# Kernel tuning notes

Measured on AMD Instinct MI355X. Metric: run time of the kernel, lower is better.

Reference implementation:

```python
import jax, jax.numpy as jnp
import numpy as np
from jax import lax

N_FFT = 1024
N_FREQ = N_FFT // 2 + 1  # 513
BATCH = 32
SAMPLES = 480000
HOP = 256


def setup_inputs() -> dict:
    key = jax.random.key(0)
    kx, kwin = jax.random.split(key)
    x = jax.random.normal(kx, (BATCH, 1, SAMPLES), dtype=jnp.float32)
    n = jnp.arange(N_FFT, dtype=jnp.float32)
    # standard rfft angular frequencies: w_k = 2*pi*k / N
    w = 2.0 * jnp.pi * jnp.arange(N_FREQ, dtype=jnp.float32) / N_FFT
    # Hann window (periodic), as typically used for STFT
    window = 0.5 - 0.5 * jnp.cos(2.0 * jnp.pi * jnp.arange(N_FFT, dtype=jnp.float32) / N_FFT)
    return {"x": x, "n": n, "w": w, "window": window, "hop_size": HOP, "power": 1}


def _create_dft_matrices(n, w, window):
    # temp[f, t] = w_f * n_t
    temp = w[:, None] * n[None, :]              # [n_freq, n_fft]
    Fr = jnp.cos(temp)
    Fi = -jnp.sin(temp)
    if window is not None:
        Fr = window * Fr
        Fi = window * Fi
    # conv1d weights: [out_ch=n_freq, in_ch=1, kernel=n_fft]
    return Fr[:, None, :], Fi[:, None, :]


def reference(x, n, w, window, hop_size, power):
    DFTr, DFTi = _create_dft_matrices(n, w, window)
    dn = ("NCH", "OIH", "NCH")
    real_x = lax.conv_general_dilated(x, DFTr, (hop_size,), "VALID", dimension_numbers=dn)
    imag_x = lax.conv_general_dilated(x, DFTi, (hop_size,), "VALID", dimension_numbers=dn)
    S = real_x ** 2 + imag_x ** 2              # [B, n_freq, n_frames]
    if not power:
        S = jnp.sqrt(S)
    return S
```

## Files before the change

### kernel.cpp

```cpp
#include <hip/hip_runtime.h>
#include <hip/hip_bf16.h>
#include <stdint.h>
#include <math.h>


#define NFFT     1024
#define NFREQ    513
#define BATCH    32
#define SAMPLES  480000
#define SAMPH    240000
#define HOPH     128
#define NFRAMES  1872
#define BN       128
#define NBPB     15
#define MBLKS    4
#define KTILES   16
#define NWG      (BATCH * NBPB * MBLKS)

#define XH_BYTES  ((size_t)BATCH * SAMPLES)
#define AWS_BYTES ((size_t)MBLKS * KTILES * 128 * 64)

#define XMAX   6.5f
#define SCALE_X (127.0f / XMAX)
#define DEQ    (XMAX / 16129.0f)
#define DEQ2   (DEQ * DEQ)

#define QX_BLOCKS 1875
#define BA_BLOCKS 2048
#define PREP_BLOCKS (QX_BLOCKS + BA_BLOCKS)

typedef __attribute__((ext_vector_type(4)))  int i32x4;
typedef __attribute__((ext_vector_type(16))) int i32x16;

#define SLOTM(r) ((((r) >> 1) & 3) ^ (((r) >> 3) & 1))

__global__ __launch_bounds__(256) void k_prep(const float* __restrict__ x,
                                              const float* __restrict__ narr,
                                              const float* __restrict__ w,
                                              const float* __restrict__ window,
                                              signed char* __restrict__ xe,
                                              signed char* __restrict__ xo,
                                              signed char* __restrict__ Aws) {
  const int bid = blockIdx.x;
  const int tid = threadIdx.x;
  if (bid < QX_BLOCKS) {
    size_t i = (size_t)bid * 256 + tid;
    const float4* x4 = (const float4*)x;
    union { signed char c[16]; uint4 v; } pe, po;
    #pragma unroll
    for (int j = 0; j < 8; ++j) {
      float4 a = x4[i * 8 + j];
      float qe  = fminf(127.f, fmaxf(-127.f, a.x * SCALE_X));
      float qo  = fminf(127.f, fmaxf(-127.f, a.y * SCALE_X));
      float qe2 = fminf(127.f, fmaxf(-127.f, a.z * SCALE_X));
      float qo2 = fminf(127.f, fmaxf(-127.f, a.w * SCALE_X));
      pe.c[j * 2]     = (signed char)__float2int_rn(qe);
      po.c[j * 2]     = (signed char)__float2int_rn(qo);
      pe.c[j * 2 + 1] = (signed char)__float2int_rn(qe2);
      po.c[j * 2 + 1] = (signed char)__float2int_rn(qo2);
    }
    ((uint4*)xe)[i] = pe.v;
    ((uint4*)xo)[i] = po.v;
  } else {
    uint32_t E = (uint32_t)(bid - QX_BLOCKS) * 256 + tid;
    uint32_t e    = E & 15;
    uint32_t s    = (E >> 4) & 3;
    uint32_t r    = (E >> 6) & 127;
    uint32_t kt   = (E >> 13) & 15;
    uint32_t mblk = E >> 17;
    uint32_t er = mblk * 128 + r;
    uint32_t j  = (kt & 7) * 64 + ((s ^ SLOTM(r)) << 4) + e;
    uint32_t odd = (kt >> 3) & 1;
    uint32_t widx = (er == 1) ? 512u : (er & ~1u);
    float ang = w[widx] * narr[j];
    float sn, cs;
    sincosf(ang, &sn, &cs);
    float base = ((er & 1) && (er != 1)) ? -sn : cs;
    float val = 127.f * window[2 * j + odd] * base;
    Aws[E] = (signed char)__float2int_rn(val);
  }
}

#define GL2LDS(g, l) __builtin_amdgcn_global_load_lds( \
    (const __attribute__((address_space(1))) uint32_t*)(g), \
    (__attribute__((address_space(3))) uint32_t*)(l), 16, 0, 0)

#define WAITV2_BAR() asm volatile("s_waitcnt vmcnt(2)\ns_barrier" ::: "memory")
#define WAIT0_BAR()  asm volatile("s_waitcnt vmcnt(0)\ns_barrier" ::: "memory")
#define LGKM0_BAR()  asm volatile("s_waitcnt lgkmcnt(0)\ns_barrier" ::: "memory")

#define SE 0
#define SO 17408
#define AR 34816

#define STAGE_STREAM(src, bl) do {                                              \
  _Pragma("unroll") for (int p_ = 0; p_ < 2; ++p_) {                            \
    int q_ = p_ * 512 + tid;                                                    \
    GL2LDS((src) + ((q_ ^ ((q_ >> 3) & 7)) << 4), &lds[(bl) + q_ * 16]);        \
  }                                                                             \
  if (tid < 64) {                                                               \
    int q_ = 1024 + tid;                                                        \
    GL2LDS((src) + ((q_ ^ ((q_ >> 3) & 7)) << 4), &lds[(bl) + q_ * 16]);        \
  }                                                                             \
} while (0)

#define STAGE_A(kt) GL2LDS(Aws + (((size_t)mblk * KTILES + (kt)) * 512 + tid) * 16, \
                           &lds[AR + ((kt) & 3) * 8192 + tid * 16])

#define READ_A2(dst, kt)                                                        \
  _Pragma("unroll") for (int mt_ = 0; mt_ < 2; ++mt_)                           \
  _Pragma("unroll") for (int ks_ = 0; ks_ < 2; ++ks_) {                         \
    int r_ = wr * 64 + mt_ * 32 + lr;                                           \
    int sl_ = (ks_ * 2 + hi) ^ SLOTM(r_);                                       \
    dst[mt_][ks_] = *(const i32x4*)&lds[AR + ((kt) & 3) * 8192 + (r_ * 4 + sl_) * 16]; \
  }

#define READ_B2(dst, ktm7, SB)                                                  \
  _Pragma("unroll") for (int ks_ = 0; ks_ < 2; ++ks_) {                         \
    int cp_ = fl * 8 + (ktm7) * 4 + 2 * ks_ + hi;                               \
    dst[ks_] = *(const i32x4*)&lds[(SB) + ((cp_ ^ ((cp_ >> 3) & 7)) << 4)];     \
  }

#define MFMA2(ACC, A_, B_) do {                                                 \
  __builtin_amdgcn_s_setprio(1);                                                \
  _Pragma("unroll") for (int ks_ = 0; ks_ < 2; ++ks_)                           \
  _Pragma("unroll") for (int mt_ = 0; mt_ < 2; ++mt_)                           \
    ACC[mt_] = __builtin_amdgcn_mfma_i32_32x32x32_i8(                           \
        A_[mt_][ks_], B_[ks_], ACC[mt_], 0, 0, 0);                              \
  __builtin_amdgcn_s_setprio(0);                                                \
  } while (0)

#define ITER(i, ACC, SB) do {                                                   \
    if ((i) == 7) WAIT0_BAR(); else WAITV2_BAR();                               \
    i32x4 a0[2][2], a1[2][2], b0[2], b1[2];                                     \
    READ_A2(a0, 2 * (i));     READ_B2(b0, (2 * (i)) & 7, SB);                   \
    READ_A2(a1, 2 * (i) + 1); READ_B2(b1, (2 * (i) + 1) & 7, SB);               \
    MFMA2(ACC, a0, b0);                                                         \
    MFMA2(ACC, a1, b1);                                                         \
    LGKM0_BAR();                                                                \
    if ((i) < 6) { STAGE_A(2 * (i) + 4); STAGE_A(2 * (i) + 5); }                \
  } while (0)

__global__ __launch_bounds__(512, 4) void k_stft(const signed char* __restrict__ xe,
                                                 const signed char* __restrict__ xo,
                                                 const signed char* __restrict__ Aws,
                                                 float* __restrict__ out) {
  __shared__ __align__(16) signed char lds[67584];
  const int tid  = threadIdx.x;
  const int lane = tid & 63;
  const int wid  = tid >> 6;
  const int wr = wid >> 2;
  const int wc = wid & 3;
  const int lr = lane & 31;
  const int hi = lane >> 5;
  const int fl = wc * 32 + lr;

  const int bx = blockIdx.x;
  const int v = (bx & 7) * 240 + (bx >> 3);
  const int mblk = v & 3;
  const int nb = v >> 2;
  const int b  = nb / NBPB;
  const int f0 = (nb - b * NBPB) * BN;

  const signed char* se_src = xe + (size_t)b * SAMPH + (size_t)f0 * HOPH;
  const signed char* so_src = xo + (size_t)b * SAMPH + (size_t)f0 * HOPH;

  i32x16 accE[2], accO[2];
  #pragma unroll
  for (int i = 0; i < 2; ++i)
    #pragma unroll
    for (int e = 0; e < 16; ++e) { accE[i][e] = 0; accO[i][e] = 0; }

  STAGE_STREAM(se_src, SE);
  STAGE_STREAM(so_src, SO);
  STAGE_A(0); STAGE_A(1); STAGE_A(2); STAGE_A(3);
  WAIT0_BAR();

  ITER(0, accE, SE); ITER(1, accE, SE); ITER(2, accE, SE); ITER(3, accE, SE);
  ITER(4, accO, SO); ITER(5, accO, SO); ITER(6, accO, SO); ITER(7, accO, SO);

  const int fbase = mblk * 64 + wr * 32;
  const int tfi = f0 + fl;
  if (tfi < NFRAMES) {
    float* op = out + (size_t)b * ((size_t)NFREQ * NFRAMES) + tfi;
    #pragma unroll
    for (int mt = 0; mt < 2; ++mt) {
      i32x16 vE = accE[mt];
      i32x16 vO = accO[mt];
      #pragma unroll
      for (int aa = 0; aa < 4; ++aa)
        #pragma unroll
        for (int q = 0; q < 2; ++q) {
          const int fq = fbase + mt * 16 + aa * 4 + 2 * hi + q;
          float Ere = (float)vE[aa * 4 + 2 * q];
          float Eim = (float)vE[aa * 4 + 2 * q + 1];
          float Ore = (float)vO[aa * 4 + 2 * q];
          float Oim = (float)vO[aa * 4 + 2 * q + 1];
          if (fq == 0) {
            float sp = Ere + Ore, sm = Ere - Ore;
            op[0]                     = DEQ2 * sp * sp;
            op[(size_t)512 * NFRAMES] = DEQ2 * sm * sm;
            op[(size_t)256 * NFRAMES] = DEQ2 * (Eim * Eim + Oim * Oim);
          } else {
            float st, ct;
            sincosf((float)fq * (float)(M_PI / 512.0), &st, &ct);
            float Pre = ct * Ore + st * Oim;
            float Pim = ct * Oim - st * Ore;
            float ar = Ere + Pre, ai = Eim + Pim;
            float br = Ere - Pre, bi = Eim - Pim;
            op[(size_t)fq * NFRAMES]         = DEQ2 * (ar * ar + ai * ai);
            op[(size_t)(512 - fq) * NFRAMES] = DEQ2 * (br * br + bi * bi);
          }
        }
    }
  }
}

extern "C" void kernel_launch(void* const* d_in, const int* in_sizes, int n_in,
                              void* d_out, int out_size, void* d_ws, size_t ws_size,
                              hipStream_t stream) {
  const float* x      = (const float*)d_in[0];
  const float* narr   = (const float*)d_in[1];
  const float* w      = (const float*)d_in[2];
  const float* window = (const float*)d_in[3];
  float* out = (float*)d_out;

  signed char* xe  = (signed char*)d_ws;
  signed char* xo  = xe + (size_t)BATCH * SAMPH;
  signed char* Aws = xo + (size_t)BATCH * SAMPH;
  if (ws_size < XH_BYTES + AWS_BYTES) return;

  k_prep<<<PREP_BLOCKS, 256, 0, stream>>>(x, narr, w, window, xe, xo, Aws);
  k_stft<<<NWG, 512, 0, stream>>>(xe, xo, Aws, out);
}
```

Measured before the change: 78.59 us.

## Use 4-wave workgroups with 2x2 MFMA tiles and precomputed twiddle table

Cuts the STFT workgroup from 8 waves to 4, so each wave computes a 2x2 grid of 32x32 MFMA tiles instead of 2x1. This increases register-level reuse of A and B fragments per LDS read. Staging loops double their per-thread loads to fill the same LDS footprint, and the stream swizzle is changed to a new XOR pattern. The per-output sincosf in the epilogue is replaced by a twiddle table that the prep kernel writes to workspace. In exchange, accumulator register pressure doubles and fewer waves are available to hide latency.

```diff
diff --git a/kernel.cpp b/kernel.cpp
--- a/kernel.cpp
+++ b/kernel.cpp
@@ -19,6 +19,7 @@
 
 #define XH_BYTES  ((size_t)BATCH * SAMPLES)
 #define AWS_BYTES ((size_t)MBLKS * KTILES * 128 * 64)
+#define TW_BYTES  (513 * 8)
 
 #define XMAX   6.5f
 #define SCALE_X (127.0f / XMAX)
@@ -27,12 +28,13 @@
 
 #define QX_BLOCKS 1875
 #define BA_BLOCKS 2048
-#define PREP_BLOCKS (QX_BLOCKS + BA_BLOCKS)
+#define PREP_BLOCKS (QX_BLOCKS + BA_BLOCKS + 1)
 
 typedef __attribute__((ext_vector_type(4)))  int i32x4;
 typedef __attribute__((ext_vector_type(16))) int i32x16;
 
 #define SLOTM(r) ((((r) >> 1) & 3) ^ (((r) >> 3) & 1))
+#define SWZ(q) ((q) ^ ((((q) >> 3) ^ ((q) >> 6)) & 7))
 
 __global__ __launch_bounds__(256) void k_prep(const float* __restrict__ x,
                                               const float* __restrict__ narr,
@@ -40,7 +42,8 @@
                                               const float* __restrict__ window,
                                               signed char* __restrict__ xe,
                                               signed char* __restrict__ xo,
-                                              signed char* __restrict__ Aws) {
+                                              signed char* __restrict__ Aws,
+                                              float2* __restrict__ tw) {
   const int bid = blockIdx.x;
   const int tid = threadIdx.x;
   if (bid < QX_BLOCKS) {
@@ -61,7 +64,7 @@
     }
     ((uint4*)xe)[i] = pe.v;
     ((uint4*)xo)[i] = po.v;
-  } else {
+  } else if (bid < QX_BLOCKS + BA_BLOCKS) {
     uint32_t E = (uint32_t)(bid - QX_BLOCKS) * 256 + tid;
     uint32_t e    = E & 15;
     uint32_t s    = (E >> 4) & 3;
@@ -78,6 +81,12 @@
     float base = ((er & 1) && (er != 1)) ? -sn : cs;
     float val = 127.f * window[2 * j + odd] * base;
     Aws[E] = (signed char)__float2int_rn(val);
+  } else {
+    for (int j = tid; j <= 512; j += 256) {
+      float st, ct;
+      sincosf((float)j * (float)(M_PI / 512.0), &st, &ct);
+      tw[j] = make_float2(ct, st);
+    }
   }
 }
 
@@ -85,7 +94,7 @@
     (const __attribute__((address_space(1))) uint32_t*)(g), \
     (__attribute__((address_space(3))) uint32_t*)(l), 16, 0, 0)
 
-#define WAITV2_BAR() asm volatile("s_waitcnt vmcnt(2)\ns_barrier" ::: "memory")
+#define WAITV4_BAR() asm volatile("s_waitcnt vmcnt(4)\ns_barrier" ::: "memory")
 #define WAIT0_BAR()  asm volatile("s_waitcnt vmcnt(0)\ns_barrier" ::: "memory")
 #define LGKM0_BAR()  asm volatile("s_waitcnt lgkmcnt(0)\ns_barrier" ::: "memory")
 
@@ -94,18 +103,22 @@
 #define AR 34816
 
 #define STAGE_STREAM(src, bl) do {                                              \
-  _Pragma("unroll") for (int p_ = 0; p_ < 2; ++p_) {                            \
-    int q_ = p_ * 512 + tid;                                                    \
-    GL2LDS((src) + ((q_ ^ ((q_ >> 3) & 7)) << 4), &lds[(bl) + q_ * 16]);        \
+  _Pragma("unroll") for (int p_ = 0; p_ < 4; ++p_) {                            \
+    int q_ = p_ * 256 + tid;                                                    \
+    GL2LDS((src) + (SWZ(q_) << 4), &lds[(bl) + q_ * 16]);                       \
   }                                                                             \
   if (tid < 64) {                                                               \
     int q_ = 1024 + tid;                                                        \
-    GL2LDS((src) + ((q_ ^ ((q_ >> 3) & 7)) << 4), &lds[(bl) + q_ * 16]);        \
+    GL2LDS((src) + (SWZ(q_) << 4), &lds[(bl) + q_ * 16]);                       \
   }                                                                             \
 } while (0)
 
-#define STAGE_A(kt) GL2LDS(Aws + (((size_t)mblk * KTILES + (kt)) * 512 + tid) * 16, \
-                           &lds[AR + ((kt) & 3) * 8192 + tid * 16])
+#define STAGE_A(kt) do {                                                        \
+  _Pragma("unroll") for (int j_ = 0; j_ < 2; ++j_) {                            \
+    int ci_ = j_ * 256 + tid;                                                   \
+    GL2LDS(Aws + (((size_t)mblk * KTILES + (kt)) * 512 + ci_) * 16,             \
+           &lds[AR + ((kt) & 3) * 8192 + ci_ * 16]);                            \
+  } } while (0)
 
 #define READ_A2(dst, kt)                                                        \
   _Pragma("unroll") for (int mt_ = 0; mt_ < 2; ++mt_)                           \
@@ -116,44 +129,46 @@
   }
 
 #define READ_B2(dst, ktm7, SB)                                                  \
+  _Pragma("unroll") for (int nt_ = 0; nt_ < 2; ++nt_)                           \
   _Pragma("unroll") for (int ks_ = 0; ks_ < 2; ++ks_) {                         \
-    int cp_ = fl * 8 + (ktm7) * 4 + 2 * ks_ + hi;                               \
-    dst[ks_] = *(const i32x4*)&lds[(SB) + ((cp_ ^ ((cp_ >> 3) & 7)) << 4)];     \
-  }
-
-#define MFMA2(ACC, A_, B_) do {                                                 \
+    int cp_ = (wc * 64 + nt_ * 32 + lr) * 8 + (ktm7) * 4 + 2 * ks_ + hi;        \
+    dst[nt_][ks_] = *(const i32x4*)&lds[(SB) + (SWZ(cp_) << 4)];                \
+  }
+
+#define MFMA8(ACC, A_, B_) do {                                                 \
   __builtin_amdgcn_s_setprio(1);                                                \
   _Pragma("unroll") for (int ks_ = 0; ks_ < 2; ++ks_)                           \
   _Pragma("unroll") for (int mt_ = 0; mt_ < 2; ++mt_)                           \
-    ACC[mt_] = __builtin_amdgcn_mfma_i32_32x32x32_i8(                           \
-        A_[mt_][ks_], B_[ks_], ACC[mt_], 0, 0, 0);                              \
+  _Pragma("unroll") for (int nt_ = 0; nt_ < 2; ++nt_)                           \
+    ACC[mt_][nt_] = __builtin_amdgcn_mfma_i32_32x32x32_i8(                      \
+        A_[mt_][ks_], B_[nt_][ks_], ACC[mt_][nt_], 0, 0, 0);                    \
   __builtin_amdgcn_s_setprio(0);                                                \
   } while (0)
 
 #define ITER(i, ACC, SB) do {                                                   \
-    if ((i) == 7) WAIT0_BAR(); else WAITV2_BAR();                               \
-    i32x4 a0[2][2], a1[2][2], b0[2], b1[2];                                     \
+    if ((i) == 7) WAIT0_BAR(); else WAITV4_BAR();                               \
+    i32x4 a0[2][2], a1[2][2], b0[2][2], b1[2][2];                               \
     READ_A2(a0, 2 * (i));     READ_B2(b0, (2 * (i)) & 7, SB);                   \
     READ_A2(a1, 2 * (i) + 1); READ_B2(b1, (2 * (i) + 1) & 7, SB);               \
-    MFMA2(ACC, a0, b0);                                                         \
-    MFMA2(ACC, a1, b1);                                                         \
+    MFMA8(ACC, a0, b0);                                                         \
+    MFMA8(ACC, a1, b1);                                                         \
     LGKM0_BAR();                                                                \
     if ((i) < 6) { STAGE_A(2 * (i) + 4); STAGE_A(2 * (i) + 5); }                \
   } while (0)
 
-__global__ __launch_bounds__(512, 4) void k_stft(const signed char* __restrict__ xe,
+__global__ __launch_bounds__(256, 2) void k_stft(const signed char* __restrict__ xe,
                                                  const signed char* __restrict__ xo,
                                                  const signed char* __restrict__ Aws,
+                                                 const float2* __restrict__ tw,
                                                  float* __restrict__ out) {
   __shared__ __align__(16) signed char lds[67584];
   const int tid  = threadIdx.x;
   const int lane = tid & 63;
   const int wid  = tid >> 6;
-  const int wr = wid >> 2;
-  const int wc = wid & 3;
+  const int wr = wid >> 1;
+  const int wc = wid & 1;
   const int lr = lane & 31;
   const int hi = lane >> 5;
-  const int fl = wc * 32 + lr;
 
   const int bx = blockIdx.x;
   const int v = (bx & 7) * 240 + (bx >> 3);
@@ -165,11 +180,13 @@
   const signed char* se_src = xe + (size_t)b * SAMPH + (size_t)f0 * HOPH;
   const signed char* so_src = xo + (size_t)b * SAMPH + (size_t)f0 * HOPH;
 
-  i32x16 accE[2], accO[2];
+  i32x16 accE[2][2], accO[2][2];
   #pragma unroll
   for (int i = 0; i < 2; ++i)
     #pragma unroll
-    for (int e = 0; e < 16; ++e) { accE[i][e] = 0; accO[i][e] = 0; }
+    for (int j = 0; j < 2; ++j)
+      #pragma unroll
+      for (int e = 0; e < 16; ++e) { accE[i][j][e] = 0; accO[i][j][e] = 0; }
 
   STAGE_STREAM(se_src, SE);
   STAGE_STREAM(so_src, SO);
@@ -180,13 +197,16 @@
   ITER(4, accO, SO); ITER(5, accO, SO); ITER(6, accO, SO); ITER(7, accO, SO);
 
   const int fbase = mblk * 64 + wr * 32;
-  const int tfi = f0 + fl;
-  if (tfi < NFRAMES) {
+  #pragma unroll
+  for (int nt = 0; nt < 2; ++nt) {
+    const int col = wc * 64 + nt * 32 + lr;
+    const int tfi = f0 + col;
+    if (tfi >= NFRAMES) continue;
     float* op = out + (size_t)b * ((size_t)NFREQ * NFRAMES) + tfi;
     #pragma unroll
     for (int mt = 0; mt < 2; ++mt) {
-      i32x16 vE = accE[mt];
-      i32x16 vO = accO[mt];
+      i32x16 vE = accE[mt][nt];
+      i32x16 vO = accO[mt][nt];
       #pragma unroll
       for (int aa = 0; aa < 4; ++aa)
         #pragma unroll
@@ -202,10 +222,9 @@
             op[(size_t)512 * NFRAMES] = DEQ2 * sm * sm;
             op[(size_t)256 * NFRAMES] = DEQ2 * (Eim * Eim + Oim * Oim);
           } else {
-            float st, ct;
-            sincosf((float)fq * (float)(M_PI / 512.0), &st, &ct);
-            float Pre = ct * Ore + st * Oim;
-            float Pim = ct * Oim - st * Ore;
+            float2 t = tw[fq];
+            float Pre = t.x * Ore + t.y * Oim;
+            float Pim = t.x * Oim - t.y * Ore;
             float ar = Ere + Pre, ai = Eim + Pim;
             float br = Ere - Pre, bi = Eim - Pim;
             op[(size_t)fq * NFRAMES]         = DEQ2 * (ar * ar + ai * ai);
@@ -228,8 +247,9 @@
   signed char* xe  = (signed char*)d_ws;
   signed char* xo  = xe + (size_t)BATCH * SAMPH;
   signed char* Aws = xo + (size_t)BATCH * SAMPH;
-  if (ws_size < XH_BYTES + AWS_BYTES) return;
-
-  k_prep<<<PREP_BLOCKS, 256, 0, stream>>>(x, narr, w, window, xe, xo, Aws);
-  k_stft<<<NWG, 512, 0, stream>>>(xe, xo, Aws, out);
+  float2*      tw  = (float2*)(Aws + AWS_BYTES);
+  if (ws_size < XH_BYTES + AWS_BYTES + TW_BYTES) return;
+
+  k_prep<<<PREP_BLOCKS, 256, 0, stream>>>(x, narr, w, window, xe, xo, Aws, tw);
+  k_stft<<<NWG, 256, 0, stream>>>(xe, xo, Aws, tw, out);
 }
```

Measured after the change: 64.47 us (median of 3 runs). 18.0% less time.
